# Performance work log

Measured on AMD Instinct MI355X. Metric: run time of the kernel, lower is better.

## Reference

```python
import jax, jax.numpy as jnp
import numpy as np

D_MODEL = 512; D_INNER = 1024; D_STATE = 16; DT_RANK = 32; D_CONV = 4
N_LAYERS = 2; LSPP = 7; N_ROI = 2048; HIDDEN = 4096


def layer_norm(x, g, b, eps=1e-5):
    mu = x.mean(-1, keepdims=True)
    v = ((x - mu) ** 2).mean(-1, keepdims=True)
    return (x - mu) * jax.lax.rsqrt(v + eps) * g + b


def causal_dwconv(u, w, b):
    # u: [N,L,Di], w: [Di,K] depthwise, causal left-pad K-1
    x = jnp.transpose(u, (0, 2, 1))
    out = jax.lax.conv_general_dilated(x, w[:, None, :], (1,), [(D_CONV - 1, 0)],
                                       dimension_numbers=('NCH', 'OIH', 'NCH'),
                                       feature_group_count=D_INNER)
    return jnp.transpose(out, (0, 2, 1)) + b


def selective_scan(u, dt, A, B, C):
    # u, dt: [N,L,Di]; B, C: [N,L,S]; A: [Di,S]
    def step(h, xs):
        dt_t, B_t, C_t, u_t = xs
        dA = jnp.exp(dt_t[..., None] * A)                      # [N,Di,S]
        h = dA * h + (dt_t * u_t)[..., None] * B_t[:, None, :]
        return h, jnp.einsum('nds,ns->nd', h, C_t)
    h0 = jnp.zeros((u.shape[0], D_INNER, D_STATE), u.dtype)
    xs = (jnp.moveaxis(dt, 1, 0), jnp.moveaxis(B, 1, 0),
          jnp.moveaxis(C, 1, 0), jnp.moveaxis(u, 1, 0))
    _, ys = jax.lax.scan(step, h0, xs)
    return jnp.moveaxis(ys, 0, 1)                              # [N,L,Di]


def mamba_block(h, inw, cw, cb, xpw, dtw, dtb, Alog, Dp, ow):
    # decomposed bidirectional mamba ('dbm'): shared in_proj/gate, fwd+bwd scans summed
    xz = h @ inw.T                                             # [N,L,2*Di]
    xi, z = jnp.split(xz, 2, axis=-1)
    ys = []
    for d in range(2):
        u = xi if d == 0 else jnp.flip(xi, axis=1)
        u = jax.nn.silu(causal_dwconv(u, cw[d], cb[d]))
        dbl = u @ xpw[d].T                                     # [N,L,DT_RANK+2S]
        dtr = dbl[..., :DT_RANK]
        B = dbl[..., DT_RANK:DT_RANK + D_STATE]
        C = dbl[..., DT_RANK + D_STATE:]
        dt = jax.nn.softplus(dtr @ dtw[d].T + dtb[d])
        A = -jnp.exp(Alog[d])
        yd = selective_scan(u, dt, A, B, C) + u * Dp[d]
        ys.append(yd if d == 0 else jnp.flip(yd, axis=1))
    return ((ys[0] + ys[1]) * jax.nn.silu(z)) @ ow.T


def setup_inputs() -> dict:
    key = jax.random.key(0)
    ks = iter(jax.random.split(key, 40))
    rn = lambda shape, scale: jax.random.normal(next(ks), shape, dtype=jnp.float32) * scale
    inp = {}
    inp['x_flat'] = rn((N_ROI, D_MODEL * LSPP), 1.0)
    inp['conv_a_w'] = rn((256, 512, 3), (512 * 3) ** -0.5)
    inp['conv_p_w'] = rn((256, 512, 1), 512 ** -0.5)
    inp['se_w1'] = rn((32, 512), 512 ** -0.5)
    inp['se_b1'] = jnp.zeros((32,), jnp.float32)
    inp['se_w2'] = rn((512, 32), 32 ** -0.5)
    inp['se_b2'] = jnp.zeros((512,), jnp.float32)
    inp['ln_g'] = jnp.ones((N_LAYERS, D_MODEL), jnp.float32)
    inp['ln_b'] = jnp.zeros((N_LAYERS, D_MODEL), jnp.float32)
    inp['in_proj_w'] = rn((N_LAYERS, 2 * D_INNER, D_MODEL), D_MODEL ** -0.5)
    inp['conv_w'] = rn((N_LAYERS, 2, D_INNER, D_CONV), D_CONV ** -0.5)
    inp['conv_b'] = jnp.zeros((N_LAYERS, 2, D_INNER), jnp.float32)
    inp['x_proj_w'] = rn((N_LAYERS, 2, DT_RANK + 2 * D_STATE, D_INNER), D_INNER ** -0.5)
    inp['dt_proj_w'] = rn((N_LAYERS, 2, D_INNER, DT_RANK), DT_RANK ** -0.5)
    inp['dt_proj_b'] = rn((N_LAYERS, 2, D_INNER), 0.1) - 4.0
    inp['A_log'] = jnp.log(jnp.arange(1., D_STATE + 1., dtype=jnp.float32)) * jnp.ones((N_LAYERS, 2, D_INNER, D_STATE), jnp.float32)
    inp['D_param'] = jnp.ones((N_LAYERS, 2, D_INNER), jnp.float32)
    inp['out_proj_w'] = rn((N_LAYERS, D_MODEL, D_INNER), D_INNER ** -0.5)
    inp['out_ln_g'] = jnp.ones((D_MODEL,), jnp.float32)
    inp['out_ln_b'] = jnp.zeros((D_MODEL,), jnp.float32)
    inp['mlp_w1'] = rn((HIDDEN, D_MODEL), D_MODEL ** -0.5)
    inp['mlp_b1'] = jnp.zeros((HIDDEN,), jnp.float32)
    inp['mlp_w2'] = rn((HIDDEN, HIDDEN), HIDDEN ** -0.5)
    inp['mlp_b2'] = jnp.zeros((HIDDEN,), jnp.float32)
    return inp


def reference(x_flat, conv_a_w, conv_p_w, se_w1, se_b1, se_w2, se_b2, ln_g, ln_b,
              in_proj_w, conv_w, conv_b, x_proj_w, dt_proj_w, dt_proj_b, A_log,
              D_param, out_proj_w, out_ln_g, out_ln_b, mlp_w1, mlp_b1, mlp_w2, mlp_b2):
    N = x_flat.shape[0]
    x = x_flat.reshape(N, D_MODEL, LSPP)                       # [N,512,7]
    dn = ('NCH', 'OIH', 'NCH')
    # TSSE: strided conv branch + maxpool branch, concat, SE gating; L: 7 -> 4
    a = jax.nn.relu(jax.lax.conv_general_dilated(x, conv_a_w, (2,), [(1, 1)], dimension_numbers=dn))
    p = jax.lax.reduce_window(x, -jnp.inf, jax.lax.max, (1, 1, 3), (1, 1, 2), ((0, 0), (0, 0), (1, 1)))
    p = jax.nn.relu(jax.lax.conv_general_dilated(p, conv_p_w, (1,), [(0, 0)], dimension_numbers=dn))
    y = jnp.concatenate([a, p], axis=1)                        # [N,512,4]
    s = jax.nn.sigmoid(jax.nn.relu(y.mean(-1) @ se_w1.T + se_b1) @ se_w2.T + se_b2)
    y = y * s[:, :, None]
    # Mamba backbone: 2 pre-norm residual DBM blocks (mask is all-ones -> no-op)
    h = jnp.transpose(y, (0, 2, 1))                            # [N,L,512]
    for l in range(N_LAYERS):
        h = h + mamba_block(layer_norm(h, ln_g[l], ln_b[l]), in_proj_w[l], conv_w[l],
                            conv_b[l], x_proj_w[l], dt_proj_w[l], dt_proj_b[l],
                            A_log[l], D_param[l], out_proj_w[l])
    h = layer_norm(h, out_ln_g, out_ln_b)
    feat = h.mean(1)                                           # mean pool over time
    z1 = jax.nn.relu(feat @ mlp_w1.T + mlp_b1)
    return jax.nn.relu(z1 @ mlp_w2.T + mlp_b2)                 # [N,4096]
```

## Files before the change

kernel.cpp:

```cpp
#include <hip/hip_runtime.h>
#include <hip/hip_bf16.h>

typedef __hip_bfloat16 bf16;
typedef __attribute__((ext_vector_type(8))) short s16x8;
typedef __attribute__((ext_vector_type(4))) float f32x4;

__device__ __forceinline__ float u2f(unsigned short u){
  union { unsigned int i; float f; } v; v.i = ((unsigned int)u) << 16; return v.f;
}
__device__ __forceinline__ float bfu(bf16 x){ return __bfloat162float(x); }
__device__ __forceinline__ bf16  f2b(float x){ return __float2bfloat16(x); }

__device__ __forceinline__ void gload16(const void* g, void* l){
  __builtin_amdgcn_global_load_lds(
      (const __attribute__((address_space(1))) void*)g,
      (__attribute__((address_space(3))) void*)l, 16, 0, 0);
}

__device__ __forceinline__ float block_sum256(float v, float* red){
  #pragma unroll
  for (int o = 32; o > 0; o >>= 1) v += __shfl_down(v, o, 64);
  int lane = threadIdx.x & 63, wid = threadIdx.x >> 6;
  if (lane == 0) red[wid] = v;
  __syncthreads();
  float r = red[0] + red[1] + red[2] + red[3];
  __syncthreads();
  return r;
}

__device__ __forceinline__ float wave_sum(float v){
  #pragma unroll
  for (int o = 1; o < 64; o <<= 1) v += __shfl_xor(v, o, 64);
  return v;
}

__device__ __forceinline__ ushort4 cvt4(float4 v){
  ushort4 o;
  o.x = __bfloat16_as_ushort(f2b(v.x));
  o.y = __bfloat16_as_ushort(f2b(v.y));
  o.z = __bfloat16_as_ushort(f2b(v.z));
  o.w = __bfloat16_as_ushort(f2b(v.w));
  return o;
}

__global__ __launch_bounds__(256) void prep_kernel(
    const float* __restrict__ caw, const float* __restrict__ cpw,
    const float* __restrict__ ipw, const float* __restrict__ opw,
    const float* __restrict__ xpw, const float* __restrict__ dtw,
    const float* __restrict__ alog,
    bf16* __restrict__ wa, bf16* __restrict__ wp,
    bf16* __restrict__ wbi, bf16* __restrict__ wbo,
    bf16* __restrict__ wxp, bf16* __restrict__ wdtp,
    float* __restrict__ atab)
{
  for (int i = blockIdx.x*256 + threadIdx.x; i < 1769472; i += gridDim.x*256){
    if (i < 917504){
      int j = i;
      const float4* src; ushort4* dst;
      if (j < 98304)      { src = (const float4*)caw; dst = (ushort4*)wa; }
      else if (j < 131072){ j -= 98304;  src = (const float4*)cpw; dst = (ushort4*)wp; }
      else if (j < 655360){ j -= 131072; src = (const float4*)ipw; dst = (ushort4*)wbi; }
      else                { j -= 655360; src = (const float4*)opw; dst = (ushort4*)wbo; }
      dst[j] = cvt4(src[j]);
    } else if (i < 1441792){
      int idx = i - 917504;
      int l = idx >> 18, rem = idx & 262143, row = rem >> 10, c = rem & 1023;
      int d = row >> 7, r = row & 127;
      float v = (r < 64) ? xpw[(((size_t)l*2 + d)*64 + r)*1024 + c] : 0.f;
      wxp[idx] = f2b(v);
    } else if (i < 1703936){
      int idx = i - 1441792;
      int ld = idx >> 16, rem = idx & 65535, r = rem >> 6, cc = rem & 63;
      float v = (cc < 32) ? dtw[((size_t)ld*1024 + r)*32 + cc] : 0.f;
      wdtp[idx] = f2b(v);
    } else {
      int idx = i - 1703936;
      atab[idx] = -__expf(alog[idx]) * 1.44269504088896f;
    }
  }
}

__global__ __launch_bounds__(256) void mlpprep_kernel(
    const float4* __restrict__ w1, const float4* __restrict__ w2,
    ushort4* __restrict__ o1, ushort4* __restrict__ o2)
{
  for (int i = blockIdx.x*256 + threadIdx.x; i < 4718592; i += gridDim.x*256){
    if (i < 524288) o1[i] = cvt4(w1[i]);
    else            o2[i - 524288] = cvt4(w2[i - 524288]);
  }
}

template<int ACT, int OMODE, bool HASBIAS>
__global__ __launch_bounds__(256) void mgemm_kernel(
    const bf16* __restrict__ A, const bf16* __restrict__ W,
    const float* __restrict__ bias, void* __restrict__ outp,
    int K, int ldo)
{
  __shared__ char lsA[16384];
  __shared__ char lsB[16384];
  const int tid = threadIdx.x;
  const int w = tid >> 6, l = tid & 63;
  const int nwg = gridDim.x * gridDim.y;
  const int lin = blockIdx.y * gridDim.x + blockIdx.x;
  const int cpx = nwg >> 3;
  const int swz = (lin & 7) * cpx + (lin >> 3);
  const int m0 = (swz % gridDim.x) * 128, n0 = (swz / gridDim.x) * 128;
  const int wr = w >> 1, wc = w & 1;
  const size_t ldb = (size_t)K * 2;
  const char* Ab = (const char*)A + (size_t)m0 * ldb;
  const char* Wb = (const char*)W + (size_t)n0 * ldb;

  const int srow = l >> 3;
  const int scb  = ((l & 7) ^ srow) << 4;
  const int fr = l & 15;
  const int fg = l >> 4;
  const int fsw = (fr & 7) << 4;

  f32x4 acc[4][4];
  #pragma unroll
  for (int m = 0; m < 4; ++m)
    #pragma unroll
    for (int n = 0; n < 4; ++n) acc[m][n] = (f32x4){0.f,0.f,0.f,0.f};

  const int nk = K >> 6;
  for (int kt = 0; kt < nk; ++kt){
    const char* As = Ab + (size_t)kt * 128;
    const char* Ws = Wb + (size_t)kt * 128;
    #pragma unroll
    for (int i = 0; i < 4; ++i){
      int row = (i*4 + w)*8 + srow;
      gload16(As + (size_t)row*ldb + scb, &lsA[(i*4 + w)*1024]);
    }
    #pragma unroll
    for (int i = 0; i < 4; ++i){
      int row = (i*4 + w)*8 + srow;
      gload16(Ws + (size_t)row*ldb + scb, &lsB[(i*4 + w)*1024]);
    }
    __syncthreads();

    s16x8 af[4][2], bfr[4][2];
    #pragma unroll
    for (int m = 0; m < 4; ++m){
      int row = wr*64 + m*16 + fr;
      af[m][0] = *(const s16x8*)&lsA[row*128 + (( 0 + fg*16) ^ fsw)];
      af[m][1] = *(const s16x8*)&lsA[row*128 + ((64 + fg*16) ^ fsw)];
    }
    #pragma unroll
    for (int n = 0; n < 4; ++n){
      int row = wc*64 + n*16 + fr;
      bfr[n][0] = *(const s16x8*)&lsB[row*128 + (( 0 + fg*16) ^ fsw)];
      bfr[n][1] = *(const s16x8*)&lsB[row*128 + ((64 + fg*16) ^ fsw)];
    }
    #pragma unroll
    for (int m = 0; m < 4; ++m)
      #pragma unroll
      for (int n = 0; n < 4; ++n){
        acc[m][n] = __builtin_amdgcn_mfma_f32_16x16x32_bf16(af[m][0], bfr[n][0], acc[m][n], 0, 0, 0);
        acc[m][n] = __builtin_amdgcn_mfma_f32_16x16x32_bf16(af[m][1], bfr[n][1], acc[m][n], 0, 0, 0);
      }
    __syncthreads();
  }

  const int orow0 = m0 + wr*64, ocol0 = n0 + wc*64;
  #pragma unroll
  for (int n = 0; n < 4; ++n){
    int col = ocol0 + n*16 + fr;
    float bv = HASBIAS ? bias[col] : 0.f;
    #pragma unroll
    for (int m = 0; m < 4; ++m){
      int rbase = orow0 + m*16 + fg*4;
      #pragma unroll
      for (int r = 0; r < 4; ++r){
        float v = acc[m][n][r] + bv;
        if (ACT == 1) v = fmaxf(v, 0.f);
        if (ACT == 2) v = (v > 20.f) ? v : log1pf(__expf(v));
        size_t oi = (size_t)(rbase + r) * ldo + col;
        if (OMODE == 0)      ((bf16*)outp)[oi] = f2b(v);
        else if (OMODE == 1) ((float*)outp)[oi] = v;
        else                 ((float*)outp)[oi] += v;
      }
    }
  }
}

template<int ACT, int OMODE, bool HASBIAS>
__global__ __launch_bounds__(256) void mgemm128_kernel(
    const bf16* __restrict__ A, const bf16* __restrict__ W,
    const float* __restrict__ bias, void* __restrict__ outp,
    int K, int ldo)
{
  __shared__ char lsA[32768];
  __shared__ char lsB[32768];
  const int tid = threadIdx.x;
  const int w = tid >> 6, l = tid & 63;
  const int nwg = gridDim.x * gridDim.y;
  const int lin = blockIdx.y * gridDim.x + blockIdx.x;
  const int cpx = nwg >> 3;
  const int swz = (lin & 7) * cpx + (lin >> 3);
  const int m0 = (swz % gridDim.x) * 128, n0 = (swz / gridDim.x) * 128;
  const int wr = w >> 1, wc = w & 1;
  const size_t ldb = (size_t)K * 2;
  const char* Ab = (const char*)A + (size_t)m0 * ldb;
  const char* Wb = (const char*)W + (size_t)n0 * ldb;

  const int srow4 = l >> 4;
  const int slot  = l & 15;
  const int fr = l & 15;
  const int fg = l >> 4;
  const int fx = fr & 7;

  f32x4 acc[4][4];
  #pragma unroll
  for (int m = 0; m < 4; ++m)
    #pragma unroll
    for (int n = 0; n < 4; ++n) acc[m][n] = (f32x4){0.f,0.f,0.f,0.f};

  const int nk = K >> 7;
  for (int kt = 0; kt < nk; ++kt){
    const char* As = Ab + (size_t)kt * 256;
    const char* Ws = Wb + (size_t)kt * 256;
    #pragma unroll
    for (int i = 0; i < 8; ++i){
      int c = i*4 + w;
      int row = c*4 + srow4;
      int colb = (slot ^ (row & 7)) << 4;
      gload16(As + (size_t)row*ldb + colb, &lsA[c*1024]);
      gload16(Ws + (size_t)row*ldb + colb, &lsB[c*1024]);
    }
    __syncthreads();

    #pragma unroll
    for (int half = 0; half < 2; ++half){
      s16x8 af[4][2], bfr[4][2];
      #pragma unroll
      for (int m = 0; m < 4; ++m){
        int row = wr*64 + m*16 + fr;
        af[m][0] = *(const s16x8*)&lsA[row*256 + ((((half*2+0)*4 + fg) ^ fx) << 4)];
        af[m][1] = *(const s16x8*)&lsA[row*256 + ((((half*2+1)*4 + fg) ^ fx) << 4)];
      }
      #pragma unroll
      for (int n = 0; n < 4; ++n){
        int row = wc*64 + n*16 + fr;
        bfr[n][0] = *(const s16x8*)&lsB[row*256 + ((((half*2+0)*4 + fg) ^ fx) << 4)];
        bfr[n][1] = *(const s16x8*)&lsB[row*256 + ((((half*2+1)*4 + fg) ^ fx) << 4)];
      }
      #pragma unroll
      for (int m = 0; m < 4; ++m)
        #pragma unroll
        for (int n = 0; n < 4; ++n){
          acc[m][n] = __builtin_amdgcn_mfma_f32_16x16x32_bf16(af[m][0], bfr[n][0], acc[m][n], 0, 0, 0);
          acc[m][n] = __builtin_amdgcn_mfma_f32_16x16x32_bf16(af[m][1], bfr[n][1], acc[m][n], 0, 0, 0);
        }
    }
    __syncthreads();
  }

  const int orow0 = m0 + wr*64, ocol0 = n0 + wc*64;
  #pragma unroll
  for (int n = 0; n < 4; ++n){
    int col = ocol0 + n*16 + fr;
    float bv = HASBIAS ? bias[col] : 0.f;
    #pragma unroll
    for (int m = 0; m < 4; ++m){
      int rbase = orow0 + m*16 + fg*4;
      #pragma unroll
      for (int r = 0; r < 4; ++r){
        float v = acc[m][n][r] + bv;
        if (ACT == 1) v = fmaxf(v, 0.f);
        if (ACT == 2) v = (v > 20.f) ? v : log1pf(__expf(v));
        size_t oi = (size_t)(rbase + r) * ldo + col;
        if (OMODE == 0)      ((bf16*)outp)[oi] = f2b(v);
        else if (OMODE == 1) ((float*)outp)[oi] = v;
        else                 ((float*)outp)[oi] += v;
      }
    }
  }
}

__global__ __launch_bounds__(256) void bgemm_kernel(
    const bf16* __restrict__ A, const bf16* __restrict__ W,
    bf16* __restrict__ dtr_buf, float* __restrict__ dbl)
{
  __shared__ char lsA[16384];
  __shared__ char lsB[16384];
  const int tid = threadIdx.x;
  const int w = tid >> 6, l = tid & 63;
  const int nwg = gridDim.x * 2;
  const int lin = blockIdx.y * gridDim.x + blockIdx.x;
  const int cpx = nwg >> 3;
  const int swz = (lin & 7) * cpx + (lin >> 3);
  const int m0 = (swz % gridDim.x) * 128;
  const int d  = swz / gridDim.x;
  const int K = 1024;
  const int wr = w >> 1, wc = w & 1;
  const size_t ldb = (size_t)K * 2;
  const char* Ab = (const char*)(A + (size_t)d*8388608) + (size_t)m0 * ldb;
  const char* Wb = (const char*)(W + (size_t)d*131072);

  const int srow = l >> 3;
  const int scb  = ((l & 7) ^ srow) << 4;
  const int fr = l & 15;
  const int fg = l >> 4;
  const int fsw = (fr & 7) << 4;

  f32x4 acc[4][4];
  #pragma unroll
  for (int m = 0; m < 4; ++m)
    #pragma unroll
    for (int n = 0; n < 4; ++n) acc[m][n] = (f32x4){0.f,0.f,0.f,0.f};

  const int nk = K >> 6;
  for (int kt = 0; kt < nk; ++kt){
    const char* As = Ab + (size_t)kt * 128;
    const char* Ws = Wb + (size_t)kt * 128;
    #pragma unroll
    for (int i = 0; i < 4; ++i){
      int row = (i*4 + w)*8 + srow;
      gload16(As + (size_t)row*ldb + scb, &lsA[(i*4 + w)*1024]);
    }
    #pragma unroll
    for (int i = 0; i < 4; ++i){
      int row = (i*4 + w)*8 + srow;
      gload16(Ws + (size_t)row*ldb + scb, &lsB[(i*4 + w)*1024]);
    }
    __syncthreads();

    s16x8 af[4][2], bfr[4][2];
    #pragma unroll
    for (int m = 0; m < 4; ++m){
      int row = wr*64 + m*16 + fr;
      af[m][0] = *(const s16x8*)&lsA[row*128 + (( 0 + fg*16) ^ fsw)];
      af[m][1] = *(const s16x8*)&lsA[row*128 + ((64 + fg*16) ^ fsw)];
    }
    #pragma unroll
    for (int n = 0; n < 4; ++n){
      int row = wc*64 + n*16 + fr;
      bfr[n][0] = *(const s16x8*)&lsB[row*128 + (( 0 + fg*16) ^ fsw)];
      bfr[n][1] = *(const s16x8*)&lsB[row*128 + ((64 + fg*16) ^ fsw)];
    }
    #pragma unroll
    for (int m = 0; m < 4; ++m)
      #pragma unroll
      for (int n = 0; n < 4; ++n){
        acc[m][n] = __builtin_amdgcn_mfma_f32_16x16x32_bf16(af[m][0], bfr[n][0], acc[m][n], 0, 0, 0);
        acc[m][n] = __builtin_amdgcn_mfma_f32_16x16x32_bf16(af[m][1], bfr[n][1], acc[m][n], 0, 0, 0);
      }
    __syncthreads();
  }

  const int orow0 = m0 + wr*64, c0 = wc*64;
  #pragma unroll
  for (int n = 0; n < 4; ++n){
    int col = c0 + n*16 + fr;
    #pragma unroll
    for (int m = 0; m < 4; ++m){
      int rbase = orow0 + m*16 + fg*4;
      #pragma unroll
      for (int r = 0; r < 4; ++r){
        float v = acc[m][n][r];
        int row = rbase + r;
        if (col < 32)
          dtr_buf[((size_t)d*8192 + row)*64 + col] = f2b(v);
        else if (col < 64)
          dbl[(size_t)row*128 + d*64 + (col - 32)] = v;
        else if (col < 96)
          dtr_buf[((size_t)d*8192 + row)*64 + (col - 32)] = f2b(v);
      }
    }
  }
}

__global__ __launch_bounds__(256) void dtgemm_kernel(
    const bf16* __restrict__ A, const bf16* __restrict__ W2,
    const float* __restrict__ bias2, bf16* __restrict__ out2)
{
  __shared__ char lsA[16384];
  __shared__ char lsB[16384];
  const int tid = threadIdx.x;
  const int w = tid >> 6, l = tid & 63;
  const int nwg = gridDim.x * gridDim.y;
  const int lin = blockIdx.y * gridDim.x + blockIdx.x;
  const int cpx = nwg >> 3;
  const int swz = (lin & 7) * cpx + (lin >> 3);
  const int m0 = (swz % gridDim.x) * 128, n0 = (swz / gridDim.x) * 128;
  const int d  = (m0 >= 8192) ? 1 : 0;
  const int wr = w >> 1, wc = w & 1;
  const size_t ldb = 128;
  const char* Ab = (const char*)A + (size_t)m0 * ldb;
  const char* Wb = (const char*)(W2 + (size_t)d*65536) + (size_t)n0 * ldb;
  const float* bias = bias2 + d*1024;
  bf16* outp = out2 + (size_t)d*8388608;

  const int srow = l >> 3;
  const int scb  = ((l & 7) ^ srow) << 4;
  const int fr = l & 15, fg = l >> 4;
  const int fsw = (fr & 7) << 4;

  f32x4 acc[4][4];
  #pragma unroll
  for (int m = 0; m < 4; ++m)
    #pragma unroll
    for (int n = 0; n < 4; ++n) acc[m][n] = (f32x4){0.f,0.f,0.f,0.f};

  #pragma unroll
  for (int i = 0; i < 4; ++i){
    int row = (i*4 + w)*8 + srow;
    gload16(Ab + (size_t)row*ldb + scb, &lsA[(i*4 + w)*1024]);
  }
  #pragma unroll
  for (int i = 0; i < 4; ++i){
    int row = (i*4 + w)*8 + srow;
    gload16(Wb + (size_t)row*ldb + scb, &lsB[(i*4 + w)*1024]);
  }
  __syncthreads();

  s16x8 af[4][2], bfr[4][2];
  #pragma unroll
  for (int m = 0; m < 4; ++m){
    int row = wr*64 + m*16 + fr;
    af[m][0] = *(const s16x8*)&lsA[row*128 + (( 0 + fg*16) ^ fsw)];
    af[m][1] = *(const s16x8*)&lsA[row*128 + ((64 + fg*16) ^ fsw)];
  }
  #pragma unroll
  for (int n = 0; n < 4; ++n){
    int row = wc*64 + n*16 + fr;
    bfr[n][0] = *(const s16x8*)&lsB[row*128 + (( 0 + fg*16) ^ fsw)];
    bfr[n][1] = *(const s16x8*)&lsB[row*128 + ((64 + fg*16) ^ fsw)];
  }
  #pragma unroll
  for (int m = 0; m < 4; ++m)
    #pragma unroll
    for (int n = 0; n < 4; ++n){
      acc[m][n] = __builtin_amdgcn_mfma_f32_16x16x32_bf16(af[m][0], bfr[n][0], acc[m][n], 0, 0, 0);
      acc[m][n] = __builtin_amdgcn_mfma_f32_16x16x32_bf16(af[m][1], bfr[n][1], acc[m][n], 0, 0, 0);
    }

  const int orow0 = (m0 - d*8192) + wr*64, ocol0 = n0 + wc*64;
  #pragma unroll
  for (int n = 0; n < 4; ++n){
    int col = ocol0 + n*16 + fr;
    float bv = bias[col];
    #pragma unroll
    for (int m = 0; m < 4; ++m){
      int rbase = orow0 + m*16 + fg*4;
      #pragma unroll
      for (int r = 0; r < 4; ++r){
        float v = acc[m][n][r] + bv;
        v = (v > 20.f) ? v : log1pf(__expf(v));
        outp[(size_t)(rbase + r) * 1024 + col] = f2b(v);
      }
    }
  }
}

__global__ __launch_bounds__(256) void im2col_kernel(
    const float* __restrict__ x_flat, bf16* __restrict__ Aa, bf16* __restrict__ P)
{
  __shared__ float xs[512][8];
  const int n = blockIdx.x, tid = threadIdx.x;
  const float* xr = x_flat + (size_t)n * 3584;
  for (int i = tid; i < 3584; i += 256) xs[i / 7][i % 7] = xr[i];
  __syncthreads();
  bf16* Ar = Aa + (size_t)n * 4 * 1536;
  for (int i = tid; i < 6144; i += 256){
    int t = i / 1536, col = i - t*1536;
    int c = col / 3, kk = col - c*3;
    int p = 2*t - 1 + kk;
    float v = (p >= 0 && p < 7) ? xs[c][p] : 0.f;
    Ar[i] = f2b(v);
  }
  bf16* Pr = P + (size_t)n * 4 * 512;
  for (int i = tid; i < 2048; i += 256){
    int t = i >> 9, c = i & 511;
    int st = 2*t - 1;
    float m = -1e30f;
    #pragma unroll
    for (int k = 0; k < 3; ++k){ int p = st + k; if (p >= 0 && p < 7) m = fmaxf(m, xs[c][p]); }
    Pr[i] = f2b(m);
  }
}

__global__ __launch_bounds__(256) void se_kernel(
    const float* __restrict__ sw1, const float* __restrict__ sb1,
    const float* __restrict__ sw2, const float* __restrict__ sb2,
    float* __restrict__ h)
{
  __shared__ float yms[512];
  __shared__ float s1s[32];
  const int n = blockIdx.x, tid = threadIdx.x;
  float* hb = h + (size_t)n * 2048;
  for (int c = tid; c < 512; c += 256)
    yms[c] = 0.25f * (hb[c] + hb[512+c] + hb[1024+c] + hb[1536+c]);
  __syncthreads();
  {
    int o = tid >> 3, sl = tid & 7;
    const float* wr = sw1 + (size_t)o * 512 + sl*64;
    const float* ym = yms + sl*64;
    float a = 0.f;
    #pragma unroll 16
    for (int i = 0; i < 64; ++i) a += wr[i] * ym[i];
    a += __shfl_down(a, 4, 8);
    a += __shfl_down(a, 2, 8);
    a += __shfl_down(a, 1, 8);
    if (sl == 0) s1s[o] = fmaxf(a + sb1[o], 0.f);
  }
  __syncthreads();
  for (int c = tid; c < 512; c += 256){
    float a = sb2[c];
    const float* wr = sw2 + (size_t)c * 32;
    #pragma unroll
    for (int j = 0; j < 32; ++j) a += wr[j] * s1s[j];
    float s = 1.f / (1.f + __expf(-a));
    #pragma unroll
    for (int t = 0; t < 4; ++t) hb[t*512 + c] *= s;
  }
}

__global__ __launch_bounds__(256) void ln_kernel(
    const float* __restrict__ x, const float* __restrict__ g,
    const float* __restrict__ b, bf16* __restrict__ out)
{
  const int lane = threadIdx.x & 63, wid = threadIdx.x >> 6;
  const int row = blockIdx.x*4 + wid;
  const float4* xr = (const float4*)(x + (size_t)row*512);
  float4 v0 = xr[lane], v1 = xr[lane + 64];
  float s = wave_sum(v0.x+v0.y+v0.z+v0.w + v1.x+v1.y+v1.z+v1.w);
  float mu = s * (1.f/512.f);
  float d0x=v0.x-mu, d0y=v0.y-mu, d0z=v0.z-mu, d0w=v0.w-mu;
  float d1x=v1.x-mu, d1y=v1.y-mu, d1z=v1.z-mu, d1w=v1.w-mu;
  float sq = wave_sum(d0x*d0x+d0y*d0y+d0z*d0z+d0w*d0w +
                      d1x*d1x+d1y*d1y+d1z*d1z+d1w*d1w);
  float rstd = rsqrtf(sq * (1.f/512.f) + 1e-5f);
  float4 g0 = ((const float4*)g)[lane], g1 = ((const float4*)g)[lane+64];
  float4 b0 = ((const float4*)b)[lane], b1 = ((const float4*)b)[lane+64];
  ushort4 o0, o1;
  o0.x = __bfloat16_as_ushort(f2b(d0x*rstd*g0.x + b0.x));
  o0.y = __bfloat16_as_ushort(f2b(d0y*rstd*g0.y + b0.y));
  o0.z = __bfloat16_as_ushort(f2b(d0z*rstd*g0.z + b0.z));
  o0.w = __bfloat16_as_ushort(f2b(d0w*rstd*g0.w + b0.w));
  o1.x = __bfloat16_as_ushort(f2b(d1x*rstd*g1.x + b1.x));
  o1.y = __bfloat16_as_ushort(f2b(d1y*rstd*g1.y + b1.y));
  o1.z = __bfloat16_as_ushort(f2b(d1z*rstd*g1.z + b1.z));
  o1.w = __bfloat16_as_ushort(f2b(d1w*rstd*g1.w + b1.w));
  ushort4* orow = (ushort4*)(out + (size_t)row*512);
  orow[lane] = o0;
  orow[lane + 64] = o1;
}

__global__ __launch_bounds__(256) void finalln_kernel(
    const float* __restrict__ h, const float* __restrict__ g,
    const float* __restrict__ b, bf16* __restrict__ feat)
{
  __shared__ float red[4];
  const int n = blockIdx.x, t = threadIdx.x;
  float a0 = 0.f, a1 = 0.f;
  for (int tt = 0; tt < 4; ++tt){
    const float* xr = h + ((size_t)n*4 + tt)*512;
    float v0 = xr[t], v1 = xr[t+256];
    float s = block_sum256(v0 + v1, red);
    float mu = s * (1.f/512.f);
    float d0 = v0 - mu, d1 = v1 - mu;
    float sq = block_sum256(d0*d0 + d1*d1, red);
    float rstd = rsqrtf(sq * (1.f/512.f) + 1e-5f);
    a0 += d0*rstd*g[t]     + b[t];
    a1 += d1*rstd*g[t+256] + b[t+256];
  }
  feat[(size_t)n*512 + t]       = f2b(a0 * 0.25f);
  feat[(size_t)n*512 + t + 256] = f2b(a1 * 0.25f);
}

__global__ __launch_bounds__(256) void dwconv2_kernel(
    const bf16* __restrict__ xz, const float* __restrict__ cw,
    const float* __restrict__ cb, bf16* __restrict__ u)
{
  const int n = blockIdx.x;
  const int c4 = threadIdx.x * 4;
  ushort4 in4[4];
  #pragma unroll
  for (int t = 0; t < 4; ++t)
    in4[t] = *reinterpret_cast<const ushort4*>(&xz[((size_t)n*4 + t)*2048 + c4]);
  #pragma unroll
  for (int d = 0; d < 2; ++d){
    const float* cwd = cw + d*4096;
    const float* cbd = cb + d*1024;
    ushort4 out[4];
    #pragma unroll
    for (int j = 0; j < 4; ++j){
      float xa[4];
      #pragma unroll
      for (int t = 0; t < 4; ++t){
        int ts = d ? 3 - t : t;
        unsigned short us = j==0?in4[ts].x : j==1?in4[ts].y : j==2?in4[ts].z : in4[ts].w;
        xa[t] = u2f(us);
      }
      float4 wv = *reinterpret_cast<const float4*>(&cwd[(c4 + j)*4]);
      float bb = cbd[c4 + j];
      float o[4];
      o[0] = xa[0]*wv.w + bb;
      o[1] = xa[0]*wv.z + xa[1]*wv.w + bb;
      o[2] = xa[0]*wv.y + xa[1]*wv.z + xa[2]*wv.w + bb;
      o[3] = xa[0]*wv.x + xa[1]*wv.y + xa[2]*wv.z + xa[3]*wv.w + bb;
      #pragma unroll
      for (int t = 0; t < 4; ++t){
        float v = o[t];
        float sv = v / (1.f + __expf(-v));
        unsigned short us = __bfloat16_as_ushort(f2b(sv));
        if (j==0) out[t].x = us; else if (j==1) out[t].y = us;
        else if (j==2) out[t].z = us; else out[t].w = us;
      }
    }
    #pragma unroll
    for (int t = 0; t < 4; ++t)
      *reinterpret_cast<ushort4*>(&u[(size_t)d*8388608 + ((size_t)n*4 + t)*1024 + c4]) = out[t];
  }
}

__global__ __launch_bounds__(256) void scan2_kernel(
    const float* __restrict__ dbl, const bf16* __restrict__ dt2,
    const bf16* __restrict__ u, const bf16* __restrict__ xz,
    const float* __restrict__ Atab2, const float* __restrict__ Dp,
    bf16* __restrict__ gated)
{
  __shared__ float Bs[2][4][16], Cs[2][4][16];
  const int n = blockIdx.x, g = blockIdx.y, tid = threadIdx.x;
  {
    int t = tid >> 6, j = tid & 63;
    int d = j >> 5, jj = j & 31;
    float v = dbl[((size_t)n*4 + t)*128 + d*64 + jj];
    if (jj < 16) Bs[d][t][jj] = v; else Cs[d][t][jj-16] = v;
  }
  __syncthreads();
  const int c = g*256 + tid;
  const size_t base = (size_t)n*4*1024 + c;
  float yo0[4], yo1[4];
  float hs[16];
  {
    float A[16];
    const float4* ap = reinterpret_cast<const float4*>(Atab2 + (size_t)c*16);
    #pragma unroll
    for (int q = 0; q < 4; ++q){
      float4 v = ap[q];
      A[q*4+0]=v.x; A[q*4+1]=v.y; A[q*4+2]=v.z; A[q*4+3]=v.w;
    }
    const float Dpc = Dp[c];
    #pragma unroll
    for (int s = 0; s < 16; ++s) hs[s] = 0.f;
    #pragma unroll
    for (int t = 0; t < 4; ++t){
      float dtv = bfu(dt2[base + (size_t)t*1024]);
      float uv  = bfu(u  [base + (size_t)t*1024]);
      float du = dtv * uv;
      float yv = 0.f;
      #pragma unroll
      for (int s = 0; s < 16; ++s){
        float dA = __builtin_amdgcn_exp2f(dtv * A[s]);
        hs[s] = dA * hs[s] + du * Bs[0][t][s];
        yv += hs[s] * Cs[0][t][s];
      }
      yo0[t] = yv + uv * Dpc;
    }
  }
  {
    float A[16];
    const float4* ap = reinterpret_cast<const float4*>(Atab2 + 16384 + (size_t)c*16);
    #pragma unroll
    for (int q = 0; q < 4; ++q){
      float4 v = ap[q];
      A[q*4+0]=v.x; A[q*4+1]=v.y; A[q*4+2]=v.z; A[q*4+3]=v.w;
    }
    const float Dpc = Dp[1024 + c];
    #pragma unroll
    for (int s = 0; s < 16; ++s) hs[s] = 0.f;
    #pragma unroll
    for (int t = 0; t < 4; ++t){
      float dtv = bfu(dt2[8388608 + base + (size_t)t*1024]);
      float uv  = bfu(u  [8388608 + base + (size_t)t*1024]);
      float du = dtv * uv;
      float yv = 0.f;
      #pragma unroll
      for (int s = 0; s < 16; ++s){
        float dA = __builtin_amdgcn_exp2f(dtv * A[s]);
        hs[s] = dA * hs[s] + du * Bs[1][t][s];
        yv += hs[s] * Cs[1][t][s];
      }
      yo1[3 - t] = yv + uv * Dpc;
    }
  }
  #pragma unroll
  for (int t = 0; t < 4; ++t){
    float z = bfu(xz[(size_t)(n*4 + t)*2048 + 1024 + c]);
    float sv = z / (1.f + __expf(-z));
    gated[base + (size_t)t*1024] = f2b((yo0[t] + yo1[t]) * sv);
  }
}

extern "C" void kernel_launch(void* const* d_in, const int* in_sizes, int n_in,
                              void* d_out, int out_size, void* d_ws, size_t ws_size,
                              hipStream_t stream)
{
  const float* x_flat    = (const float*)d_in[0];
  const float* conv_a_w  = (const float*)d_in[1];
  const float* conv_p_w  = (const float*)d_in[2];
  const float* se_w1     = (const float*)d_in[3];
  const float* se_b1     = (const float*)d_in[4];
  const float* se_w2     = (const float*)d_in[5];
  const float* se_b2     = (const float*)d_in[6];
  const float* ln_g      = (const float*)d_in[7];
  const float* ln_b      = (const float*)d_in[8];
  const float* in_proj_w = (const float*)d_in[9];
  const float* conv_w    = (const float*)d_in[10];
  const float* conv_b    = (const float*)d_in[11];
  const float* x_proj_w  = (const float*)d_in[12];
  const float* dt_proj_w = (const float*)d_in[13];
  const float* dt_proj_b = (const float*)d_in[14];
  const float* A_log     = (const float*)d_in[15];
  const float* D_param   = (const float*)d_in[16];
  const float* out_proj_w= (const float*)d_in[17];
  const float* out_ln_g  = (const float*)d_in[18];
  const float* out_ln_b  = (const float*)d_in[19];
  const float* mlp_w1    = (const float*)d_in[20];
  const float* mlp_b1    = (const float*)d_in[21];
  const float* mlp_w2    = (const float*)d_in[22];
  const float* mlp_b2    = (const float*)d_in[23];

  char* ws = (char*)d_ws;
  const size_t OFF_H    = 0;
  const size_t OFF_HN   = OFF_H    + 16777216;
  const size_t OFF_XZ   = OFF_HN   + 8388608;
  const size_t OFF_U    = OFF_XZ   + 33554432;
  const size_t OFF_SCR  = OFF_U    + 33554432;
  const size_t OFF_YB   = OFF_SCR  + 25165824;
  const size_t OFF_WB   = OFF_YB   + 33554432;
  const size_t OFF_WXP  = OFF_WB   + 6291456;
  const size_t OFF_WDT  = OFF_WXP  + 1048576;
  const size_t OFF_ATAB = OFF_WDT  + 524288;

  float* h    = (float*)(ws + OFF_H);
  bf16*  hn   = (bf16*) (ws + OFF_HN);
  bf16*  xz   = (bf16*) (ws + OFF_XZ);
  bf16*  u    = (bf16*) (ws + OFF_U);
  float* dbl  = (float*)(ws + OFF_SCR);
  bf16*  dtrb = (bf16*) (ws + OFF_SCR + 4194304);
  bf16*  dt2  = (bf16*) (ws + OFF_YB);
  bf16*  feat = (bf16*) (ws + OFF_HN);
  bf16*  z1   = (bf16*) (ws + OFF_XZ);
  bf16*  wbi  = (bf16*) (ws + OFF_WB);
  bf16*  wbo  = (bf16*) (ws + OFF_WB + 4194304);
  bf16*  wxp  = (bf16*) (ws + OFF_WXP);
  bf16*  wdtp = (bf16*) (ws + OFF_WDT);
  float* Atab = (float*)(ws + OFF_ATAB);
  bf16*  wb1  = (bf16*) (ws + OFF_SCR);
  bf16*  wb2  = (bf16*) (ws + OFF_YB);
  bf16*  Aa   = (bf16*) (ws + OFF_SCR);
  bf16*  Pm   = (bf16*) (ws + OFF_YB);
  bf16*  wa   = (bf16*) (ws + OFF_YB + 8388608);
  bf16*  wp   = (bf16*) (ws + OFF_YB + 8388608 + 786432);
  float* outf = (float*)d_out;

  prep_kernel<<<2048, 256, 0, stream>>>(
      conv_a_w, conv_p_w, in_proj_w, out_proj_w, x_proj_w, dt_proj_w, A_log,
      wa, wp, wbi, wbo, wxp, wdtp, Atab);

  im2col_kernel<<<2048, 256, 0, stream>>>(x_flat, Aa, Pm);
  mgemm_kernel<1,1,false><<<dim3(64,2), 256, 0, stream>>>(
      Aa, wa, nullptr, h, 1536, 512);
  mgemm_kernel<1,1,false><<<dim3(64,2), 256, 0, stream>>>(
      Pm, wp, nullptr, (float*)h + 256, 512, 512);
  se_kernel<<<2048, 256, 0, stream>>>(se_w1, se_b1, se_w2, se_b2, h);

  for (int l = 0; l < 2; ++l){
    ln_kernel<<<2048, 256, 0, stream>>>(h, ln_g + l*512, ln_b + l*512, hn);
    mgemm_kernel<0,0,false><<<dim3(64,16), 256, 0, stream>>>(
        hn, wbi + (size_t)l*2048*512, nullptr, xz, 512, 2048);
    dwconv2_kernel<<<2048, 256, 0, stream>>>(
        xz, conv_w + (size_t)l*8192, conv_b + (size_t)l*2048, u);
    bgemm_kernel<<<dim3(64,2), 256, 0, stream>>>(
        u, wxp + (size_t)l*262144, dtrb, dbl);
    dtgemm_kernel<<<dim3(128,8), 256, 0, stream>>>(
        dtrb, wdtp + (size_t)l*131072, dt_proj_b + (size_t)l*2048, dt2);
    scan2_kernel<<<dim3(2048,4), 256, 0, stream>>>(
        dbl, dt2, u, xz, Atab + (size_t)l*32768, D_param + (size_t)l*2048,
        u );
    mgemm128_kernel<0,2,false><<<dim3(64,4), 256, 0, stream>>>(
        u, wbo + (size_t)l*512*1024, nullptr, h, 1024, 512);
  }

  finalln_kernel<<<2048, 256, 0, stream>>>(h, out_ln_g, out_ln_b, feat);

  mlpprep_kernel<<<4096, 256, 0, stream>>>(
      (const float4*)mlp_w1, (const float4*)mlp_w2, (ushort4*)wb1, (ushort4*)wb2);

  mgemm128_kernel<1,0,true><<<dim3(16,32), 256, 0, stream>>>(
      feat, wb1, mlp_b1, z1, 512, 4096);
  mgemm128_kernel<1,1,true><<<dim3(16,32), 256, 0, stream>>>(
      z1, wb2, mlp_b2, outf, 4096, 4096);
}
```

Measured before the change: 653.6 us.

## Merge prep/im2col, stem GEMMs, SE+LN, and final LN+MLP weight conversion kernels

Cuts the launch count with several fusions. Weight conversion now shares one launch with im2col, and the final layer norm shares one with the MLP weight conversion, split by block index. The two stem conv GEMMs become a single stemgemm kernel over a 64x4 grid, and the first layer's LayerNorm is folded into the SE kernel. This removes launches and one round trip of h through memory, but makes the merged kernels heterogeneous, so slow blocks of one part can delay the whole launch.

After: 636.8 us (median of 2 runs). 2.6% less time.

```diff
diff --git a/kernel.cpp b/kernel.cpp
--- a/kernel.cpp
+++ b/kernel.cpp
@@ -15,17 +15,6 @@
   __builtin_amdgcn_global_load_lds(
       (const __attribute__((address_space(1))) void*)g,
       (__attribute__((address_space(3))) void*)l, 16, 0, 0);
-}
-
-__device__ __forceinline__ float block_sum256(float v, float* red){
-  #pragma unroll
-  for (int o = 32; o > 0; o >>= 1) v += __shfl_down(v, o, 64);
-  int lane = threadIdx.x & 63, wid = threadIdx.x >> 6;
-  if (lane == 0) red[wid] = v;
-  __syncthreads();
-  float r = red[0] + red[1] + red[2] + red[3];
-  __syncthreads();
-  return r;
 }
 
 __device__ __forceinline__ float wave_sum(float v){
@@ -43,50 +32,68 @@
   return o;
 }
 
-__global__ __launch_bounds__(256) void prep_kernel(
+__global__ __launch_bounds__(256) void prep_im2col_kernel(
+    const float* __restrict__ x_flat,
     const float* __restrict__ caw, const float* __restrict__ cpw,
     const float* __restrict__ ipw, const float* __restrict__ opw,
     const float* __restrict__ xpw, const float* __restrict__ dtw,
     const float* __restrict__ alog,
+    bf16* __restrict__ Aa, bf16* __restrict__ P,
     bf16* __restrict__ wa, bf16* __restrict__ wp,
     bf16* __restrict__ wbi, bf16* __restrict__ wbo,
     bf16* __restrict__ wxp, bf16* __restrict__ wdtp,
     float* __restrict__ atab)
 {
-  for (int i = blockIdx.x*256 + threadIdx.x; i < 1769472; i += gridDim.x*256){
-    if (i < 917504){
-      int j = i;
-      const float4* src; ushort4* dst;
-      if (j < 98304)      { src = (const float4*)caw; dst = (ushort4*)wa; }
-      else if (j < 131072){ j -= 98304;  src = (const float4*)cpw; dst = (ushort4*)wp; }
-      else if (j < 655360){ j -= 131072; src = (const float4*)ipw; dst = (ushort4*)wbi; }
-      else                { j -= 655360; src = (const float4*)opw; dst = (ushort4*)wbo; }
-      dst[j] = cvt4(src[j]);
-    } else if (i < 1441792){
-      int idx = i - 917504;
-      int l = idx >> 18, rem = idx & 262143, row = rem >> 10, c = rem & 1023;
-      int d = row >> 7, r = row & 127;
-      float v = (r < 64) ? xpw[(((size_t)l*2 + d)*64 + r)*1024 + c] : 0.f;
-      wxp[idx] = f2b(v);
-    } else if (i < 1703936){
-      int idx = i - 1441792;
-      int ld = idx >> 16, rem = idx & 65535, r = rem >> 6, cc = rem & 63;
-      float v = (cc < 32) ? dtw[((size_t)ld*1024 + r)*32 + cc] : 0.f;
-      wdtp[idx] = f2b(v);
-    } else {
-      int idx = i - 1703936;
-      atab[idx] = -__expf(alog[idx]) * 1.44269504088896f;
-    }
-  }
-}
-
-__global__ __launch_bounds__(256) void mlpprep_kernel(
-    const float4* __restrict__ w1, const float4* __restrict__ w2,
-    ushort4* __restrict__ o1, ushort4* __restrict__ o2)
-{
-  for (int i = blockIdx.x*256 + threadIdx.x; i < 4718592; i += gridDim.x*256){
-    if (i < 524288) o1[i] = cvt4(w1[i]);
-    else            o2[i - 524288] = cvt4(w2[i - 524288]);
+  __shared__ float xs[512][8];
+  const int tid = threadIdx.x;
+  if (blockIdx.x < 2048){
+    const int n = blockIdx.x;
+    const float* xr = x_flat + (size_t)n * 3584;
+    for (int i = tid; i < 3584; i += 256) xs[i / 7][i % 7] = xr[i];
+    __syncthreads();
+    bf16* Ar = Aa + (size_t)n * 4 * 1536;
+    for (int i = tid; i < 6144; i += 256){
+      int t = i / 1536, col = i - t*1536;
+      int c = col / 3, kk = col - c*3;
+      int p = 2*t - 1 + kk;
+      float v = (p >= 0 && p < 7) ? xs[c][p] : 0.f;
+      Ar[i] = f2b(v);
+    }
+    bf16* Pr = P + (size_t)n * 4 * 512;
+    for (int i = tid; i < 2048; i += 256){
+      int t = i >> 9, c = i & 511;
+      int st = 2*t - 1;
+      float m = -1e30f;
+      #pragma unroll
+      for (int k = 0; k < 3; ++k){ int p = st + k; if (p >= 0 && p < 7) m = fmaxf(m, xs[c][p]); }
+      Pr[i] = f2b(m);
+    }
+  } else {
+    for (int i = (blockIdx.x - 2048)*256 + tid; i < 1769472; i += 2048*256){
+      if (i < 917504){
+        int j = i;
+        const float4* src; ushort4* dst;
+        if (j < 98304)      { src = (const float4*)caw; dst = (ushort4*)wa; }
+        else if (j < 131072){ j -= 98304;  src = (const float4*)cpw; dst = (ushort4*)wp; }
+        else if (j < 655360){ j -= 131072; src = (const float4*)ipw; dst = (ushort4*)wbi; }
+        else                { j -= 655360; src = (const float4*)opw; dst = (ushort4*)wbo; }
+        dst[j] = cvt4(src[j]);
+      } else if (i < 1441792){
+        int idx = i - 917504;
+        int l = idx >> 18, rem = idx & 262143, row = rem >> 10, c = rem & 1023;
+        int d = row >> 7, r = row & 127;
+        float v = (r < 64) ? xpw[(((size_t)l*2 + d)*64 + r)*1024 + c] : 0.f;
+        wxp[idx] = f2b(v);
+      } else if (i < 1703936){
+        int idx = i - 1441792;
+        int ld = idx >> 16, rem = idx & 65535, r = rem >> 6, cc = rem & 63;
+        float v = (cc < 32) ? dtw[((size_t)ld*1024 + r)*32 + cc] : 0.f;
+        wdtp[idx] = f2b(v);
+      } else {
+        int idx = i - 1703936;
+        atab[idx] = -__expf(alog[idx]) * 1.44269504088896f;
+      }
+    }
   }
 }
 
@@ -179,6 +186,94 @@
         else if (OMODE == 1) ((float*)outp)[oi] = v;
         else                 ((float*)outp)[oi] += v;
       }
+    }
+  }
+}
+
+__global__ __launch_bounds__(256) void stemgemm_kernel(
+    const bf16* __restrict__ Aa, const bf16* __restrict__ wa,
+    const bf16* __restrict__ Pm, const bf16* __restrict__ wp,
+    float* __restrict__ h)
+{
+  __shared__ char lsA[16384];
+  __shared__ char lsB[16384];
+  const int tid = threadIdx.x;
+  const int w = tid >> 6, l = tid & 63;
+  const int lin = blockIdx.y * gridDim.x + blockIdx.x;
+  const int swz = (lin & 7) * 32 + (lin >> 3);
+  const int tm = swz & 63, ty = swz >> 6;
+  const int m0 = tm * 128;
+  const bf16* A;
+  const bf16* W;
+  int K;
+  if (ty < 2){ A = Aa; W = wa + (size_t)(ty)*128*1536; K = 1536; }
+  else       { A = Pm; W = wp + (size_t)(ty-2)*128*512; K = 512; }
+  const int wr = w >> 1, wc = w & 1;
+  const size_t ldb = (size_t)K * 2;
+  const char* Ab = (const char*)A + (size_t)m0 * ldb;
+  const char* Wb = (const char*)W;
+
+  const int srow = l >> 3;
+  const int scb  = ((l & 7) ^ srow) << 4;
+  const int fr = l & 15;
+  const int fg = l >> 4;
+  const int fsw = (fr & 7) << 4;
+
+  f32x4 acc[4][4];
+  #pragma unroll
+  for (int m = 0; m < 4; ++m)
+    #pragma unroll
+    for (int n = 0; n < 4; ++n) acc[m][n] = (f32x4){0.f,0.f,0.f,0.f};
+
+  const int nk = K >> 6;
+  for (int kt = 0; kt < nk; ++kt){
+    const char* As = Ab + (size_t)kt * 128;
+    const char* Ws = Wb + (size_t)kt * 128;
+    #pragma unroll
+    for (int i = 0; i < 4; ++i){
+      int row = (i*4 + w)*8 + srow;
+      gload16(As + (size_t)row*ldb + scb, &lsA[(i*4 + w)*1024]);
+    }
+    #pragma unroll
+    for (int i = 0; i < 4; ++i){
+      int row = (i*4 + w)*8 + srow;
+      gload16(Ws + (size_t)row*ldb + scb, &lsB[(i*4 + w)*1024]);
+    }
+    __syncthreads();
+
+    s16x8 af[4][2], bfr[4][2];
+    #pragma unroll
+    for (int m = 0; m < 4; ++m){
+      int row = wr*64 + m*16 + fr;
+      af[m][0] = *(const s16x8*)&lsA[row*128 + (( 0 + fg*16) ^ fsw)];
+      af[m][1] = *(const s16x8*)&lsA[row*128 + ((64 + fg*16) ^ fsw)];
+    }
+    #pragma unroll
+    for (int n = 0; n < 4; ++n){
+      int row = wc*64 + n*16 + fr;
+      bfr[n][0] = *(const s16x8*)&lsB[row*128 + (( 0 + fg*16) ^ fsw)];
+      bfr[n][1] = *(const s16x8*)&lsB[row*128 + ((64 + fg*16) ^ fsw)];
+    }
+    #pragma unroll
+    for (int m = 0; m < 4; ++m)
+      #pragma unroll
+      for (int n = 0; n < 4; ++n){
+        acc[m][n] = __builtin_amdgcn_mfma_f32_16x16x32_bf16(af[m][0], bfr[n][0], acc[m][n], 0, 0, 0);
+        acc[m][n] = __builtin_amdgcn_mfma_f32_16x16x32_bf16(af[m][1], bfr[n][1], acc[m][n], 0, 0, 0);
+      }
+    __syncthreads();
+  }
+
+  const int orow0 = m0 + wr*64, ocol0 = ty*128 + wc*64;
+  #pragma unroll
+  for (int n = 0; n < 4; ++n){
+    int col = ocol0 + n*16 + fr;
+    #pragma unroll
+    for (int m = 0; m < 4; ++m){
+      int rbase = orow0 + m*16 + fg*4;
+      #pragma unroll
+      for (int r = 0; r < 4; ++r)
+        h[(size_t)(rbase + r)*512 + col] = fmaxf(acc[m][n][r], 0.f);
     }
   }
 }
@@ -453,40 +548,15 @@
   }
 }
 
-__global__ __launch_bounds__(256) void im2col_kernel(
-    const float* __restrict__ x_flat, bf16* __restrict__ Aa, bf16* __restrict__ P)
-{
-  __shared__ float xs[512][8];
-  const int n = blockIdx.x, tid = threadIdx.x;
-  const float* xr = x_flat + (size_t)n * 3584;
-  for (int i = tid; i < 3584; i += 256) xs[i / 7][i % 7] = xr[i];
-  __syncthreads();
-  bf16* Ar = Aa + (size_t)n * 4 * 1536;
-  for (int i = tid; i < 6144; i += 256){
-    int t = i / 1536, col = i - t*1536;
-    int c = col / 3, kk = col - c*3;
-    int p = 2*t - 1 + kk;
-    float v = (p >= 0 && p < 7) ? xs[c][p] : 0.f;
-    Ar[i] = f2b(v);
-  }
-  bf16* Pr = P + (size_t)n * 4 * 512;
-  for (int i = tid; i < 2048; i += 256){
-    int t = i >> 9, c = i & 511;
-    int st = 2*t - 1;
-    float m = -1e30f;
-    #pragma unroll
-    for (int k = 0; k < 3; ++k){ int p = st + k; if (p >= 0 && p < 7) m = fmaxf(m, xs[c][p]); }
-    Pr[i] = f2b(m);
-  }
-}
-
-__global__ __launch_bounds__(256) void se_kernel(
+__global__ __launch_bounds__(256) void se_ln_kernel(
     const float* __restrict__ sw1, const float* __restrict__ sb1,
     const float* __restrict__ sw2, const float* __restrict__ sb2,
-    float* __restrict__ h)
+    const float* __restrict__ g, const float* __restrict__ b,
+    float* __restrict__ h, bf16* __restrict__ hn)
 {
   __shared__ float yms[512];
   __shared__ float s1s[32];
+  __shared__ float sg[512];
   const int n = blockIdx.x, tid = threadIdx.x;
   float* hb = h + (size_t)n * 2048;
   for (int c = tid; c < 512; c += 256)
@@ -510,10 +580,38 @@
     const float* wr = sw2 + (size_t)c * 32;
     #pragma unroll
     for (int j = 0; j < 32; ++j) a += wr[j] * s1s[j];
-    float s = 1.f / (1.f + __expf(-a));
-    #pragma unroll
-    for (int t = 0; t < 4; ++t) hb[t*512 + c] *= s;
-  }
+    sg[c] = 1.f / (1.f + __expf(-a));
+  }
+  __syncthreads();
+  const int lane = tid & 63, wv = tid >> 6;
+  float* hr = hb + wv*512;
+  float4 v0 = ((float4*)hr)[lane], v1 = ((float4*)hr)[lane + 64];
+  int c0 = lane*4, c1 = 256 + lane*4;
+  v0.x *= sg[c0+0]; v0.y *= sg[c0+1]; v0.z *= sg[c0+2]; v0.w *= sg[c0+3];
+  v1.x *= sg[c1+0]; v1.y *= sg[c1+1]; v1.z *= sg[c1+2]; v1.w *= sg[c1+3];
+  ((float4*)hr)[lane] = v0;
+  ((float4*)hr)[lane + 64] = v1;
+  float s = wave_sum(v0.x+v0.y+v0.z+v0.w + v1.x+v1.y+v1.z+v1.w);
+  float mu = s * (1.f/512.f);
+  float d0x=v0.x-mu, d0y=v0.y-mu, d0z=v0.z-mu, d0w=v0.w-mu;
+  float d1x=v1.x-mu, d1y=v1.y-mu, d1z=v1.z-mu, d1w=v1.w-mu;
+  float sq = wave_sum(d0x*d0x+d0y*d0y+d0z*d0z+d0w*d0w +
+                      d1x*d1x+d1y*d1y+d1z*d1z+d1w*d1w);
+  float rstd = rsqrtf(sq * (1.f/512.f) + 1e-5f);
+  float4 g0 = ((const float4*)g)[lane], g1 = ((const float4*)g)[lane+64];
+  float4 b0 = ((const float4*)b)[lane], b1 = ((const float4*)b)[lane+64];
+  ushort4 o0, o1;
+  o0.x = __bfloat16_as_ushort(f2b(d0x*rstd*g0.x + b0.x));
+  o0.y = __bfloat16_as_ushort(f2b(d0y*rstd*g0.y + b0.y));
+  o0.z = __bfloat16_as_ushort(f2b(d0z*rstd*g0.z + b0.z));
+  o0.w = __bfloat16_as_ushort(f2b(d0w*rstd*g0.w + b0.w));
+  o1.x = __bfloat16_as_ushort(f2b(d1x*rstd*g1.x + b1.x));
+  o1.y = __bfloat16_as_ushort(f2b(d1y*rstd*g1.y + b1.y));
+  o1.z = __bfloat16_as_ushort(f2b(d1z*rstd*g1.z + b1.z));
+  o1.w = __bfloat16_as_ushort(f2b(d1w*rstd*g1.w + b1.w));
+  ushort4* orow = (ushort4*)(hn + ((size_t)n*4 + wv)*512);
+  orow[lane] = o0;
+  orow[lane + 64] = o1;
 }
 
 __global__ __launch_bounds__(256) void ln_kernel(
@@ -547,26 +645,49 @@
   orow[lane + 64] = o1;
 }
 
-__global__ __launch_bounds__(256) void finalln_kernel(
+__global__ __launch_bounds__(256) void finalln_mlp_kernel(
     const float* __restrict__ h, const float* __restrict__ g,
-    const float* __restrict__ b, bf16* __restrict__ feat)
+    const float* __restrict__ b, bf16* __restrict__ feat,
+    const float4* __restrict__ w1, const float4* __restrict__ w2,
+    ushort4* __restrict__ o1, ushort4* __restrict__ o2)
 {
   __shared__ float red[4];
-  const int n = blockIdx.x, t = threadIdx.x;
-  float a0 = 0.f, a1 = 0.f;
-  for (int tt = 0; tt < 4; ++tt){
-    const float* xr = h + ((size_t)n*4 + tt)*512;
-    float v0 = xr[t], v1 = xr[t+256];
-    float s = block_sum256(v0 + v1, red);
-    float mu = s * (1.f/512.f);
-    float d0 = v0 - mu, d1 = v1 - mu;
-    float sq = block_sum256(d0*d0 + d1*d1, red);
-    float rstd = rsqrtf(sq * (1.f/512.f) + 1e-5f);
-    a0 += d0*rstd*g[t]     + b[t];
-    a1 += d1*rstd*g[t+256] + b[t+256];
-  }
-  feat[(size_t)n*512 + t]       = f2b(a0 * 0.25f);
-  feat[(size_t)n*512 + t + 256] = f2b(a1 * 0.25f);
+  const int tid = threadIdx.x;
+  if (blockIdx.x < 2048){
+    const int n = blockIdx.x, t = tid;
+    float a0 = 0.f, a1 = 0.f;
+    for (int tt = 0; tt < 4; ++tt){
+      const float* xr = h + ((size_t)n*4 + tt)*512;
+      float v0 = xr[t], v1 = xr[t+256];
+      float sv = v0 + v1;
+      #pragma unroll
+      for (int o = 32; o > 0; o >>= 1) sv += __shfl_down(sv, o, 64);
+      int lane = tid & 63, wid = tid >> 6;
+      if (lane == 0) red[wid] = sv;
+      __syncthreads();
+      float s = red[0] + red[1] + red[2] + red[3];
+      __syncthreads();
+      float mu = s * (1.f/512.f);
+      float d0 = v0 - mu, d1 = v1 - mu;
+      float q = d0*d0 + d1*d1;
+      #pragma unroll
+      for (int o = 32; o > 0; o >>= 1) q += __shfl_down(q, o, 64);
+      if (lane == 0) red[wid] = q;
+      __syncthreads();
+      float sq = red[0] + red[1] + red[2] + red[3];
+      __syncthreads();
+      float rstd = rsqrtf(sq * (1.f/512.f) + 1e-5f);
+      a0 += d0*rstd*g[t]     + b[t];
+      a1 += d1*rstd*g[t+256] + b[t+256];
+    }
+    feat[(size_t)n*512 + t]       = f2b(a0 * 0.25f);
+    feat[(size_t)n*512 + t + 256] = f2b(a1 * 0.25f);
+  } else {
+    for (int i = (blockIdx.x - 2048)*256 + tid; i < 4718592; i += 4096*256){
+      if (i < 524288) o1[i] = cvt4(w1[i]);
+      else            o2[i - 524288] = cvt4(w2[i - 524288]);
+    }
+  }
 }
 
 __global__ __launch_bounds__(256) void dwconv2_kernel(
@@ -757,19 +878,18 @@
   bf16*  wp   = (bf16*) (ws + OFF_YB + 8388608 + 786432);
   float* outf = (float*)d_out;
 
-  prep_kernel<<<2048, 256, 0, stream>>>(
-      conv_a_w, conv_p_w, in_proj_w, out_proj_w, x_proj_w, dt_proj_w, A_log,
-      wa, wp, wbi, wbo, wxp, wdtp, Atab);
-
-  im2col_kernel<<<2048, 256, 0, stream>>>(x_flat, Aa, Pm);
-  mgemm_kernel<1,1,false><<<dim3(64,2), 256, 0, stream>>>(
-      Aa, wa, nullptr, h, 1536, 512);
-  mgemm_kernel<1,1,false><<<dim3(64,2), 256, 0, stream>>>(
-      Pm, wp, nullptr, (float*)h + 256, 512, 512);
-  se_kernel<<<2048, 256, 0, stream>>>(se_w1, se_b1, se_w2, se_b2, h);
+  prep_im2col_kernel<<<4096, 256, 0, stream>>>(
+      x_flat, conv_a_w, conv_p_w, in_proj_w, out_proj_w, x_proj_w, dt_proj_w,
+      A_log, Aa, Pm, wa, wp, wbi, wbo, wxp, wdtp, Atab);
+
+  stemgemm_kernel<<<dim3(64,4), 256, 0, stream>>>(Aa, wa, Pm, wp, h);
+
+  se_ln_kernel<<<2048, 256, 0, stream>>>(
+      se_w1, se_b1, se_w2, se_b2, ln_g, ln_b, h, hn);
 
   for (int l = 0; l < 2; ++l){
-    ln_kernel<<<2048, 256, 0, stream>>>(h, ln_g + l*512, ln_b + l*512, hn);
+    if (l == 1)
+      ln_kernel<<<2048, 256, 0, stream>>>(h, ln_g + 512, ln_b + 512, hn);
     mgemm_kernel<0,0,false><<<dim3(64,16), 256, 0, stream>>>(
         hn, wbi + (size_t)l*2048*512, nullptr, xz, 512, 2048);
     dwconv2_kernel<<<2048, 256, 0, stream>>>(
@@ -785,9 +905,8 @@
         u, wbo + (size_t)l*512*1024, nullptr, h, 1024, 512);
   }
 
-  finalln_kernel<<<2048, 256, 0, stream>>>(h, out_ln_g, out_ln_b, feat);
-
-  mlpprep_kernel<<<4096, 256, 0, stream>>>(
+  finalln_mlp_kernel<<<6144, 256, 0, stream>>>(
+      h, out_ln_g, out_ln_b, feat,
       (const float4*)mlp_w1, (const float4*)mlp_w2, (ushort4*)wb1, (ushort4*)wb2);
 
   mgemm128_kernel<1,0,true><<<dim3(16,32), 256, 0, stream>>>(
```
